# Kernel tuning notes

Measured on AMD Instinct MI355X. Metric: run time of the kernel, lower is better.

Reference implementation:

```python
import jax, jax.numpy as jnp
import numpy as np
from jax import lax

WINDOW_SIZE = 7
SIGMA = 1.5
C1 = 0.01 ** 2
C2 = 0.03 ** 2


def gaussian_window3d(window_size: int, channel: int) -> jnp.ndarray:
    g = jnp.arange(window_size, dtype=jnp.float32) - window_size // 2
    g = jnp.exp(-g ** 2 / (2.0 * SIGMA ** 2))
    g = g / g.sum()  # [k]
    w3 = g[:, None, None] * g[None, :, None] * g[None, None, :]  # [k,k,k]
    # OIDHW layout for depthwise conv: [channel, 1, k, k, k]
    return jnp.broadcast_to(w3[None, None], (channel, 1, window_size, window_size, window_size))


def depthwise_conv3d(x, window):
    # x: [N,C,D,H,W]; window: [C,1,k,k,k]; SAME padding via pad = k//2
    k = window.shape[-1]
    p = k // 2
    return lax.conv_general_dilated(
        x, window,
        window_strides=(1, 1, 1),
        padding=[(p, p)] * 3,
        dimension_numbers=('NCDHW', 'OIDHW', 'NCDHW'),
        feature_group_count=x.shape[1],
    )


def setup_inputs() -> dict:
    key = jax.random.key(0)
    k1, k2 = jax.random.split(key)
    shape = (2, 1, 160, 256, 256)
    img1 = jax.random.uniform(k1, shape, dtype=jnp.float32)
    img2 = jax.random.uniform(k2, shape, dtype=jnp.float32)
    window = gaussian_window3d(WINDOW_SIZE, shape[1])
    return {"img1": img1, "img2": img2, "window": window}


def reference(img1, img2, window):
    mu1 = depthwise_conv3d(img1, window)
    mu2 = depthwise_conv3d(img2, window)
    mu1_sq = mu1 * mu1
    mu2_sq = mu2 * mu2
    mu1_mu2 = mu1 * mu2
    sigma1_sq = depthwise_conv3d(img1 * img1, window) - mu1_sq
    sigma2_sq = depthwise_conv3d(img2 * img2, window) - mu2_sq
    sigma12 = depthwise_conv3d(img1 * img2, window) - mu1_mu2
    ssim_map = ((2.0 * mu1_mu2 + C1) * (2.0 * sigma12 + C2)) / (
        (mu1_sq + mu2_sq + C1) * (sigma1_sq + sigma2_sq + C2)
    )
    return ssim_map.mean()  # size_average=True
```

## Files before the change

### kernel.cpp

```cpp
#include <hip/hip_runtime.h>
#include <math.h>

#define HW 65536
#define DD 160
#define NB 2
#define DCH 80
#define NSL (DCH + 6)

#define SSIM_C1 1e-4f
#define SSIM_C2 9e-4f

struct Gw { float g[7]; };

__global__ __launch_bounds__(512) void k_fused(
    const float* __restrict__ img1, const float* __restrict__ img2,
    Gw gw, float* __restrict__ partials)
{
    __shared__ float sx[38][41];
    __shared__ float sy[38][41];
    __shared__ float b1[5][38][33];
    __shared__ float red[512];

    const int tid = threadIdx.x;
    const int n  = blockIdx.z >> 1;
    const int o0 = (blockIdx.z & 1) * DCH;
    const int h0 = blockIdx.y * 32;
    const int w0 = blockIdx.x * 32;
    const float* i1 = img1 + (size_t)n * DD * HW;
    const float* i2 = img2 + (size_t)n * DD * HW;

    int goff[3], loff[3];
    bool ok[3], wr[3];
#pragma unroll
    for (int q = 0; q < 3; ++q) {
        int idx = tid + 512 * q;
        int hh = idx / 38;
        int ww = idx - 38 * hh;
        int gh = h0 - 3 + hh;
        int gw2 = w0 - 3 + ww;
        wr[q] = (idx < 1444);
        ok[q] = wr[q] && ((unsigned)gh < 256u) && ((unsigned)gw2 < 256u);
        goff[q] = gh * 256 + gw2;
        loff[q] = hh * 41 + ww;
    }

    const int wcol = tid & 31;
    const int hb = (tid >> 5) * 2;

    float ring[2][5][7] = {};
    float lsum = 0.f;

    float* sxf = &sx[0][0];
    float* syf = &sy[0][0];

    {
        int s0 = o0 - 3;
        if (s0 >= 0) {
            const float* p1 = i1 + (size_t)s0 * HW;
            const float* p2 = i2 + (size_t)s0 * HW;
#pragma unroll
            for (int q = 0; q < 3; ++q) {
                float vx = ok[q] ? p1[goff[q]] : 0.f;
                float vy = ok[q] ? p2[goff[q]] : 0.f;
                if (wr[q]) { sxf[loff[q]] = vx; syf[loff[q]] = vy; }
            }
        }
        __syncthreads();
    }

    for (int t = 0; t < 13; ++t) {
#pragma unroll
        for (int p = 0; p < 7; ++p) {
            const int r = 7 * t + p;
            if (r < NSL) {
                const int s = o0 - 3 + r;
                const bool curv = (s >= 0 && s < DD);
                const int sn = s + 1;
                const bool nxtv = (r + 1 < NSL) && (sn >= 0) && (sn < DD);

                float pfx[3], pfy[3];
                if (nxtv) {
                    const float* p1 = i1 + (size_t)sn * HW;
                    const float* p2 = i2 + (size_t)sn * HW;
#pragma unroll
                    for (int q = 0; q < 3; ++q) {
                        pfx[q] = ok[q] ? p1[goff[q]] : 0.f;
                        pfy[q] = ok[q] ? p2[goff[q]] : 0.f;
                    }
                }

                if (curv && tid < 304) {
                    const int hh = tid >> 3;
                    const int wb = (tid & 7) * 4;
                    float xv[10], yv[10], pxx[10], pyy[10], pxy[10];
#pragma unroll
                    for (int i = 0; i < 10; ++i) { xv[i] = sx[hh][wb + i]; yv[i] = sy[hh][wb + i]; }
#pragma unroll
                    for (int i = 0; i < 10; ++i) {
                        pxx[i] = xv[i] * xv[i]; pyy[i] = yv[i] * yv[i]; pxy[i] = xv[i] * yv[i];
                    }
                    float a[4][5] = {};
#pragma unroll
                    for (int k = 0; k < 7; ++k) {
                        const float gk = gw.g[k];
#pragma unroll
                        for (int o = 0; o < 4; ++o) {
                            const int i = o + k;
                            a[o][0] += gk * xv[i];
                            a[o][1] += gk * yv[i];
                            a[o][2] += gk * pxx[i];
                            a[o][3] += gk * pyy[i];
                            a[o][4] += gk * pxy[i];
                        }
                    }
#pragma unroll
                    for (int f = 0; f < 5; ++f)
#pragma unroll
                        for (int o = 0; o < 4; ++o) b1[f][hh][wb + o] = a[o][f];
                }
                __syncthreads();

                if (nxtv) {
#pragma unroll
                    for (int q = 0; q < 3; ++q)
                        if (wr[q]) { sxf[loff[q]] = pfx[q]; syf[loff[q]] = pfy[q]; }
                }

                if (curv) {
#pragma unroll
                    for (int f = 0; f < 5; ++f) {
                        float v[8];
#pragma unroll
                        for (int i = 0; i < 8; ++i) v[i] = b1[f][hb + i][wcol];
#pragma unroll
                        for (int o = 0; o < 2; ++o) {
                            float acc = 0.f;
#pragma unroll
                            for (int k = 0; k < 7; ++k) acc += gw.g[k] * v[o + k];
                            ring[o][f][p] = acc;
                        }
                    }
                } else {
#pragma unroll
                    for (int o = 0; o < 2; ++o)
#pragma unroll
                        for (int f = 0; f < 5; ++f) ring[o][f][p] = 0.f;
                }

                if (r >= 6) {
#pragma unroll
                    for (int o = 0; o < 2; ++o) {
                        float c0 = 0.f, c1 = 0.f, c2 = 0.f, c3 = 0.f, c4 = 0.f;
#pragma unroll
                        for (int k = 0; k < 7; ++k) {
                            const float gk = gw.g[k];
                            const int pp = (p + 1 + k) % 7;
                            c0 += gk * ring[o][0][pp];
                            c1 += gk * ring[o][1][pp];
                            c2 += gk * ring[o][2][pp];
                            c3 += gk * ring[o][3][pp];
                            c4 += gk * ring[o][4][pp];
                        }
                        const float mu1 = c0, mu2 = c1;
                        const float mu1s = mu1 * mu1, mu2s = mu2 * mu2, m12 = mu1 * mu2;
                        const float s1 = c2 - mu1s, s2 = c3 - mu2s, s12 = c4 - m12;
                        const float num = (2.f * m12 + SSIM_C1) * (2.f * s12 + SSIM_C2);
                        const float den = (mu1s + mu2s + SSIM_C1) * (s1 + s2 + SSIM_C2);
                        lsum += num / den;
                    }
                }
                __syncthreads();
            }
        }
    }

    red[tid] = lsum;
    __syncthreads();
    for (int off = 256; off > 0; off >>= 1) {
        if (tid < off) red[tid] += red[tid + off];
        __syncthreads();
    }
    if (tid == 0)
        partials[(blockIdx.z * gridDim.y + blockIdx.y) * gridDim.x + blockIdx.x] = red[0];
}

__global__ __launch_bounds__(256) void k_final(
    const float* __restrict__ partials, int n, float scale, float* __restrict__ out)
{
    __shared__ float red[256];
    float s = 0.f;
    for (int i = threadIdx.x; i < n; i += 256) s += partials[i];
    red[threadIdx.x] = s;
    __syncthreads();
    for (int off = 128; off > 0; off >>= 1) {
        if (threadIdx.x < off) red[threadIdx.x] += red[threadIdx.x + off];
        __syncthreads();
    }
    if (threadIdx.x == 0) out[0] = red[0] * scale;
}

extern "C" void kernel_launch(void* const* d_in, const int* in_sizes, int n_in,
                              void* d_out, int out_size, void* d_ws, size_t ws_size,
                              hipStream_t stream)
{
    const float* img1 = (const float*)d_in[0];
    const float* img2 = (const float*)d_in[1];
    float* out = (float*)d_out;
    float* partials = (float*)d_ws;

    Gw gw;
    {
        double gs[7], sum = 0.0;
        for (int i = 0; i < 7; ++i) { double x = i - 3; gs[i] = exp(-x * x / 4.5); sum += gs[i]; }
        for (int i = 0; i < 7; ++i) gw.g[i] = (float)(gs[i] / sum);
    }

    dim3 grid(8, 8, NB * 2);
    k_fused<<<grid, dim3(512), 0, stream>>>(img1, img2, gw, partials);
    k_final<<<dim3(1), dim3(256), 0, stream>>>(
        partials, 8 * 8 * NB * 2, (float)(1.0 / 20971520.0), out);
}
```

Before: 186.5 us.

## Load halo slices into registers and double-buffer W-pass output to halve barriers

```diff
diff --git a/kernel.cpp b/kernel.cpp
--- a/kernel.cpp
+++ b/kernel.cpp
@@ -6,42 +6,43 @@
 #define NB 2
 #define DCH 80
 #define NSL (DCH + 6)
+#define NCH 2
 
 #define SSIM_C1 1e-4f
 #define SSIM_C2 9e-4f
 
 struct Gw { float g[7]; };
 
-__global__ __launch_bounds__(512) void k_fused(
+__global__ __launch_bounds__(512, 2) void k_fused(
     const float* __restrict__ img1, const float* __restrict__ img2,
     Gw gw, float* __restrict__ partials)
 {
-    __shared__ float sx[38][41];
-    __shared__ float sy[38][41];
-    __shared__ float b1[5][38][33];
+    __shared__ float b1t[2][5][32][42];
     __shared__ float red[512];
 
     const int tid = threadIdx.x;
-    const int n  = blockIdx.z >> 1;
+    const int nb = blockIdx.z >> 1;
     const int o0 = (blockIdx.z & 1) * DCH;
     const int h0 = blockIdx.y * 32;
     const int w0 = blockIdx.x * 32;
-    const float* i1 = img1 + (size_t)n * DD * HW;
-    const float* i2 = img2 + (size_t)n * DD * HW;
-
-    int goff[3], loff[3];
-    bool ok[3], wr[3];
-#pragma unroll
-    for (int q = 0; q < 3; ++q) {
-        int idx = tid + 512 * q;
-        int hh = idx / 38;
-        int ww = idx - 38 * hh;
-        int gh = h0 - 3 + hh;
-        int gw2 = w0 - 3 + ww;
-        wr[q] = (idx < 1444);
-        ok[q] = wr[q] && ((unsigned)gh < 256u) && ((unsigned)gw2 < 256u);
-        goff[q] = gh * 256 + gw2;
-        loff[q] = hh * 41 + ww;
+    const float* i1 = img1 + (size_t)nb * DD * HW;
+    const float* i2 = img2 + (size_t)nb * DD * HW;
+
+    const int hh = tid >> 3;
+    const int wb = (tid & 7) * 4;
+    const int gh = h0 - 3 + hh;
+    const int gwb = w0 - 3 + wb;
+    const bool wth = (tid < 304);
+    const bool ghv = wth && ((unsigned)gh < 256u);
+    const int ghc = gh < 0 ? 0 : (gh > 255 ? 255 : gh);
+    int coff[10];
+    float msk[10];
+#pragma unroll
+    for (int i = 0; i < 10; ++i) {
+        int gwi = gwb + i;
+        int gc = gwi < 0 ? 0 : (gwi > 255 ? 255 : gwi);
+        coff[i] = ghc * 256 + gc;
+        msk[i] = (ghv && gwi == gc) ? 1.f : 0.f;
     }
 
     const int wcol = tid & 31;
@@ -49,124 +50,124 @@
 
     float ring[2][5][7] = {};
     float lsum = 0.f;
-
-    float* sxf = &sx[0][0];
-    float* syf = &sy[0][0];
+    float cx[10], cy[10];
 
     {
-        int s0 = o0 - 3;
-        if (s0 >= 0) {
+        const int s0 = o0 - 3;
+        if (s0 >= 0 && wth) {
             const float* p1 = i1 + (size_t)s0 * HW;
             const float* p2 = i2 + (size_t)s0 * HW;
 #pragma unroll
-            for (int q = 0; q < 3; ++q) {
-                float vx = ok[q] ? p1[goff[q]] : 0.f;
-                float vy = ok[q] ? p2[goff[q]] : 0.f;
-                if (wr[q]) { sxf[loff[q]] = vx; syf[loff[q]] = vy; }
+            for (int i = 0; i < 10; ++i) {
+                cx[i] = p1[coff[i]] * msk[i];
+                cy[i] = p2[coff[i]] * msk[i];
             }
         }
-        __syncthreads();
     }
 
     for (int t = 0; t < 13; ++t) {
 #pragma unroll
         for (int p = 0; p < 7; ++p) {
             const int r = 7 * t + p;
-            if (r < NSL) {
-                const int s = o0 - 3 + r;
-                const bool curv = (s >= 0 && s < DD);
-                const int sn = s + 1;
-                const bool nxtv = (r + 1 < NSL) && (sn >= 0) && (sn < DD);
-
-                float pfx[3], pfy[3];
-                if (nxtv) {
-                    const float* p1 = i1 + (size_t)sn * HW;
-                    const float* p2 = i2 + (size_t)sn * HW;
-#pragma unroll
-                    for (int q = 0; q < 3; ++q) {
-                        pfx[q] = ok[q] ? p1[goff[q]] : 0.f;
-                        pfy[q] = ok[q] ? p2[goff[q]] : 0.f;
-                    }
-                }
-
-                if (curv && tid < 304) {
-                    const int hh = tid >> 3;
-                    const int wb = (tid & 7) * 4;
-                    float xv[10], yv[10], pxx[10], pyy[10], pxy[10];
-#pragma unroll
-                    for (int i = 0; i < 10; ++i) { xv[i] = sx[hh][wb + i]; yv[i] = sy[hh][wb + i]; }
+            if (r <= NSL) {
+                const int scur = o0 - 3 + r;
+                const bool wv = (r < NSL) && (scur >= 0) && (scur < DD);
+                const int snx = scur + 1;
+                const bool pfv = (r + 1 < NSL) && (snx >= 0) && (snx < DD);
+
+                float pfx[10], pfy[10];
+                if (pfv && wth) {
+                    const float* p1 = i1 + (size_t)snx * HW;
+                    const float* p2 = i2 + (size_t)snx * HW;
+#pragma unroll
+                    for (int i = 0; i < 10; ++i) pfx[i] = p1[coff[i]];
+#pragma unroll
+                    for (int i = 0; i < 10; ++i) pfy[i] = p2[coff[i]];
+                }
+
+                if (wv && wth) {
+                    float a[4][5] = {};
 #pragma unroll
                     for (int i = 0; i < 10; ++i) {
-                        pxx[i] = xv[i] * xv[i]; pyy[i] = yv[i] * yv[i]; pxy[i] = xv[i] * yv[i];
-                    }
-                    float a[4][5] = {};
-#pragma unroll
-                    for (int k = 0; k < 7; ++k) {
-                        const float gk = gw.g[k];
+                        const float xx = cx[i] * cx[i];
+                        const float yy = cy[i] * cy[i];
+                        const float xy = cx[i] * cy[i];
 #pragma unroll
                         for (int o = 0; o < 4; ++o) {
-                            const int i = o + k;
-                            a[o][0] += gk * xv[i];
-                            a[o][1] += gk * yv[i];
-                            a[o][2] += gk * pxx[i];
-                            a[o][3] += gk * pyy[i];
-                            a[o][4] += gk * pxy[i];
+                            const int k = i - o;
+                            if (k >= 0 && k < 7) {
+                                const float gk = gw.g[k];
+                                a[o][0] += gk * cx[i];
+                                a[o][1] += gk * cy[i];
+                                a[o][2] += gk * xx;
+                                a[o][3] += gk * yy;
+                                a[o][4] += gk * xy;
+                            }
                         }
                     }
+                    float* bb = &b1t[r & 1][0][0][0];
 #pragma unroll
                     for (int f = 0; f < 5; ++f)
 #pragma unroll
-                        for (int o = 0; o < 4; ++o) b1[f][hh][wb + o] = a[o][f];
-                }
-                __syncthreads();
-
-                if (nxtv) {
-#pragma unroll
-                    for (int q = 0; q < 3; ++q)
-                        if (wr[q]) { sxf[loff[q]] = pfx[q]; syf[loff[q]] = pfy[q]; }
-                }
-
-                if (curv) {
-#pragma unroll
-                    for (int f = 0; f < 5; ++f) {
-                        float v[8];
-#pragma unroll
-                        for (int i = 0; i < 8; ++i) v[i] = b1[f][hb + i][wcol];
+                        for (int o = 0; o < 4; ++o)
+                            bb[f * (32 * 42) + (wb + o) * 42 + hh] = a[o][f];
+                }
+
+                if (r >= 1) {
+                    const int rp = r - 1;
+                    const int sp = o0 - 3 + rp;
+                    const int pi = (p + 6) % 7;
+                    if (sp >= 0 && sp < DD) {
+                        const float* br = &b1t[rp & 1][0][0][0];
+#pragma unroll
+                        for (int f = 0; f < 5; ++f) {
+                            float v[8];
+#pragma unroll
+                            for (int i = 0; i < 8; ++i)
+                                v[i] = br[f * (32 * 42) + wcol * 42 + hb + i];
+#pragma unroll
+                            for (int o = 0; o < 2; ++o) {
+                                float acc = 0.f;
+#pragma unroll
+                                for (int k = 0; k < 7; ++k) acc += gw.g[k] * v[o + k];
+                                ring[o][f][pi] = acc;
+                            }
+                        }
+                    } else {
+#pragma unroll
+                        for (int o = 0; o < 2; ++o)
+#pragma unroll
+                            for (int f = 0; f < 5; ++f) ring[o][f][pi] = 0.f;
+                    }
+                    if (r >= 7) {
 #pragma unroll
                         for (int o = 0; o < 2; ++o) {
-                            float acc = 0.f;
-#pragma unroll
-                            for (int k = 0; k < 7; ++k) acc += gw.g[k] * v[o + k];
-                            ring[o][f][p] = acc;
+                            float c0 = 0.f, c1 = 0.f, c2 = 0.f, c3 = 0.f, c4 = 0.f;
+#pragma unroll
+                            for (int k = 0; k < 7; ++k) {
+                                const float gk = gw.g[k];
+                                const int pp = (pi + 1 + k) % 7;
+                                c0 += gk * ring[o][0][pp];
+                                c1 += gk * ring[o][1][pp];
+                                c2 += gk * ring[o][2][pp];
+                                c3 += gk * ring[o][3][pp];
+                                c4 += gk * ring[o][4][pp];
+                            }
+                            const float mu1 = c0, mu2 = c1;
+                            const float mu1s = mu1 * mu1, mu2s = mu2 * mu2, m12 = mu1 * mu2;
+                            const float s1 = c2 - mu1s, s2 = c3 - mu2s, s12 = c4 - m12;
+                            const float num = (2.f * m12 + SSIM_C1) * (2.f * s12 + SSIM_C2);
+                            const float den = (mu1s + mu2s + SSIM_C1) * (s1 + s2 + SSIM_C2);
+                            lsum += num / den;
                         }
                     }
-                } else {
-#pragma unroll
-                    for (int o = 0; o < 2; ++o)
-#pragma unroll
-                        for (int f = 0; f < 5; ++f) ring[o][f][p] = 0.f;
-                }
-
-                if (r >= 6) {
-#pragma unroll
-                    for (int o = 0; o < 2; ++o) {
-                        float c0 = 0.f, c1 = 0.f, c2 = 0.f, c3 = 0.f, c4 = 0.f;
-#pragma unroll
-                        for (int k = 0; k < 7; ++k) {
-                            const float gk = gw.g[k];
-                            const int pp = (p + 1 + k) % 7;
-                            c0 += gk * ring[o][0][pp];
-                            c1 += gk * ring[o][1][pp];
-                            c2 += gk * ring[o][2][pp];
-                            c3 += gk * ring[o][3][pp];
-                            c4 += gk * ring[o][4][pp];
-                        }
-                        const float mu1 = c0, mu2 = c1;
-                        const float mu1s = mu1 * mu1, mu2s = mu2 * mu2, m12 = mu1 * mu2;
-                        const float s1 = c2 - mu1s, s2 = c3 - mu2s, s12 = c4 - m12;
-                        const float num = (2.f * m12 + SSIM_C1) * (2.f * s12 + SSIM_C2);
-                        const float den = (mu1s + mu2s + SSIM_C1) * (s1 + s2 + SSIM_C2);
-                        lsum += num / den;
+                }
+
+                if (pfv && wth) {
+#pragma unroll
+                    for (int i = 0; i < 10; ++i) {
+                        cx[i] = pfx[i] * msk[i];
+                        cy[i] = pfy[i] * msk[i];
                     }
                 }
                 __syncthreads();
@@ -215,8 +216,8 @@
         for (int i = 0; i < 7; ++i) gw.g[i] = (float)(gs[i] / sum);
     }
 
-    dim3 grid(8, 8, NB * 2);
+    dim3 grid(8, 8, NB * NCH);
     k_fused<<<grid, dim3(512), 0, stream>>>(img1, img2, gw, partials);
     k_final<<<dim3(1), dim3(256), 0, stream>>>(
-        partials, 8 * 8 * NB * 2, (float)(1.0 / 20971520.0), out);
+        partials, 8 * 8 * NB * NCH, (float)(1.0 / 20971520.0), out);
 }
```

New measurement: 207.5 us. +11.3%, slower.
